# Performance work log

Measured on AMD Instinct MI355X. Metric: run time of the kernel, lower is better.

## Reference

```python
import jax, jax.numpy as jnp
import numpy as np

N = 500_000      # active voxels
G = 128          # grid extent per axis
CIN, COUT = 32, 64
KK = 27          # 3x3x3 kernel offsets
EPS = 1e-5


def setup_inputs() -> dict:
    rng = np.random.default_rng(0)
    # unique active voxel coordinates in a G^3 grid
    lin = rng.choice(G ** 3, size=N, replace=False)
    coords = np.stack(np.unravel_index(lin, (G, G, G)), -1).astype(np.int64)  # [N,3]
    lut = np.full(G ** 3, N, np.int64)  # N == "missing" sentinel
    lut[lin] = np.arange(N)
    offs = np.stack(np.meshgrid(*([np.arange(-1, 2)] * 3), indexing='ij'), -1).reshape(-1, 3)
    nbr = np.full((N, KK), N, np.int64)  # kernel map: nbr[i,k] = input index at coord_i + off_k
    for k, o in enumerate(offs):
        c = coords + o
        valid = np.all((c >= 0) & (c < G), axis=1)
        keys = (c[:, 0] * G + c[:, 1]) * G + c[:, 2]
        nbr[valid, k] = lut[keys[valid]]

    key = jax.random.key(0)
    ks = jax.random.split(key, 4)
    x = jax.random.normal(ks[0], (N, CIN), jnp.float32)
    W1 = jax.random.normal(ks[1], (KK, CIN, COUT), jnp.float32) * (1.0 / np.sqrt(KK * CIN))
    W2 = jax.random.normal(ks[2], (KK, COUT, COUT), jnp.float32) * (1.0 / np.sqrt(KK * COUT))
    Wres = jax.random.normal(ks[3], (CIN, COUT), jnp.float32) * (1.0 / np.sqrt(CIN))
    bres = jnp.zeros((COUT,), jnp.float32)
    g1 = jnp.ones((CIN,), jnp.float32)
    b1 = jnp.zeros((CIN,), jnp.float32)
    g2 = jnp.ones((COUT,), jnp.float32)
    b2 = jnp.zeros((COUT,), jnp.float32)
    return dict(x=x, nbr=jnp.asarray(nbr), W1=W1, W2=W2, Wres=Wres, bres=bres,
                g1=g1, b1=b1, g2=g2, b2=b2)


def _bn(x, g, b):
    # MinkowskiBatchNorm (training mode): stats over all active sites
    m = jnp.mean(x, axis=0)
    v = jnp.var(x, axis=0)
    return (x - m) * jax.lax.rsqrt(v + EPS) * g + b


def _sparse_conv(x, nbr, W):
    # gather-GEMM-scatter sparse conv; x:[N,Cin], nbr:[N,KK], W:[KK,Cin,Cout]
    xp = jnp.concatenate([x, jnp.zeros((1, x.shape[1]), x.dtype)], axis=0)  # sentinel row
    out = jnp.zeros((x.shape[0], W.shape[2]), x.dtype)
    for k in range(W.shape[0]):  # fixed small loop over 27 kernel offsets
        out = out + xp[nbr[:, k]] @ W[k]
    return out


def reference(x, nbr, W1, W2, Wres, bres, g1, b1, g2, b2):
    residual = x @ Wres + bres                               # MinkowskiLinear (in != out)
    out = _sparse_conv(jax.nn.relu(_bn(x, g1, b1)), nbr, W1)   # conv1(act1(norm1(x)))
    out = _sparse_conv(jax.nn.relu(_bn(out, g2, b2)), nbr, W2)  # conv2(act2(norm2(out)))
    return out + residual
```

## Files before the change

### kernel.cpp

```cpp
#include <hip/hip_runtime.h>

#define NVOX 500000
#define CIN 32
#define COUT 64
#define KK 27
#define EPSV 1e-5f

typedef __bf16 bf16x8 __attribute__((ext_vector_type(8)));
typedef float f32x4 __attribute__((ext_vector_type(4)));

#define MFMA16 __builtin_amdgcn_mfma_f32_16x16x32_bf16

__device__ __forceinline__ float bf2f(ushort u) {
    return __uint_as_float(((unsigned)u) << 16);
}
__device__ __forceinline__ ushort f2bf(float f) {
    unsigned u = __float_as_uint(f);
    unsigned r = (u + 0x7FFFu + ((u >> 16) & 1u)) >> 16;
    return (ushort)r;
}
union U4BF { uint4 u; bf16x8 b; ushort s[8]; };
__device__ __forceinline__ bf16x8 as_bf8(uint4 v) { U4BF c; c.u = v; return c.b; }
__device__ __forceinline__ bf16x8 f8_to_bf8(float4 a, float4 b) {
    U4BF c;
    c.s[0] = f2bf(a.x); c.s[1] = f2bf(a.y); c.s[2] = f2bf(a.z); c.s[3] = f2bf(a.w);
    c.s[4] = f2bf(b.x); c.s[5] = f2bf(b.y); c.s[6] = f2bf(b.z); c.s[7] = f2bf(b.w);
    return c.b;
}

__device__ __forceinline__ float4 ldv4(const float4* p, long long i) { return p[i]; }
__device__ __forceinline__ float4 ldv4(const ushort4* p, long long i) {
    ushort4 u = p[i];
    return make_float4(bf2f(u.x), bf2f(u.y), bf2f(u.z), bf2f(u.w));
}

__global__ void prep_kernel(const float* __restrict__ W1, const float* __restrict__ W2,
                            const float* __restrict__ Wres,
                            ushort* __restrict__ w1s, ushort* __restrict__ w2s,
                            ushort* __restrict__ wrs,
                            float* __restrict__ stats,
                            ushort* __restrict__ y1, ushort* __restrict__ y2) {
    int t = blockIdx.x * 256 + threadIdx.x;
    if (t < 192) { stats[t] = 0.f; return; }
    if (t < 224) { y1[(size_t)NVOX * CIN + (t - 192)] = 0; return; }
    if (t < 288) { y2[(size_t)NVOX * COUT + (t - 224)] = 0; return; }
    int d = t - 288;
    if (d < 27 * 4 * 64 * 8) {
        int j = d & 7, lane = (d >> 3) & 63, nt = (d >> 9) & 3, k = d >> 11;
        int ci = ((lane >> 4) << 3) + j, co = (nt << 4) + (lane & 15);
        w1s[d] = f2bf(W1[(k * CIN + ci) * COUT + co]);
        return;
    }
    d -= 27 * 4 * 64 * 8;
    if (d < 27 * 2 * 4 * 64 * 8) {
        int j = d & 7, lane = (d >> 3) & 63, nt = (d >> 9) & 3, half = (d >> 11) & 1, k = d >> 12;
        int ci = (half << 5) + ((lane >> 4) << 3) + j, co = (nt << 4) + (lane & 15);
        w2s[d] = f2bf(W2[(k * COUT + ci) * COUT + co]);
        return;
    }
    d -= 27 * 2 * 4 * 64 * 8;
    if (d < 4 * 64 * 8) {
        int j = d & 7, lane = (d >> 3) & 63, nt = (d >> 9) & 3;
        int ci = ((lane >> 4) << 3) + j, co = (nt << 4) + (lane & 15);
        wrs[d] = f2bf(Wres[ci * COUT + co]);
    }
}

template <int C, typename T4>
__global__ void stats_kernel(const T4* __restrict__ in, long long total4,
                             float* __restrict__ gsum, float* __restrict__ gsq) {
    __shared__ float s_sum[C];
    __shared__ float s_sq[C];
    int t = threadIdx.x;
    if (t < C) { s_sum[t] = 0.f; s_sq[t] = 0.f; }
    __syncthreads();
    long long i0 = (long long)blockIdx.x * blockDim.x + t;
    long long stride = (long long)gridDim.x * blockDim.x;
    int c0 = (int)((i0 * 4) & (C - 1));
    float ls0 = 0.f, ls1 = 0.f, ls2 = 0.f, ls3 = 0.f;
    float lq0 = 0.f, lq1 = 0.f, lq2 = 0.f, lq3 = 0.f;
    for (long long i = i0; i < total4; i += stride) {
        float4 v = ldv4(in, i);
        ls0 += v.x; lq0 += v.x * v.x;
        ls1 += v.y; lq1 += v.y * v.y;
        ls2 += v.z; lq2 += v.z * v.z;
        ls3 += v.w; lq3 += v.w * v.w;
    }
    atomicAdd(&s_sum[c0 + 0], ls0); atomicAdd(&s_sq[c0 + 0], lq0);
    atomicAdd(&s_sum[c0 + 1], ls1); atomicAdd(&s_sq[c0 + 1], lq1);
    atomicAdd(&s_sum[c0 + 2], ls2); atomicAdd(&s_sq[c0 + 2], lq2);
    atomicAdd(&s_sum[c0 + 3], ls3); atomicAdd(&s_sq[c0 + 3], lq3);
    __syncthreads();
    if (t < C) {
        atomicAdd(&gsum[t], s_sum[t]);
        atomicAdd(&gsq[t], s_sq[t]);
    }
}

template <int C, typename T4>
__global__ void bn_relu_kernel(const T4* __restrict__ in, ushort4* __restrict__ out,
                               long long total4,
                               const float* __restrict__ gsum, const float* __restrict__ gsq,
                               const float* __restrict__ gamma, const float* __restrict__ beta,
                               float invN) {
    long long i0 = (long long)blockIdx.x * blockDim.x + threadIdx.x;
    long long stride = (long long)gridDim.x * blockDim.x;
    int c0 = (int)((i0 * 4) & (C - 1));
    float a[4], bb[4];
#pragma unroll
    for (int j = 0; j < 4; j++) {
        int c = c0 + j;
        float m = gsum[c] * invN;
        float v = fmaxf(gsq[c] * invN - m * m, 0.f);
        a[j] = gamma[c] * rsqrtf(v + EPSV);
        bb[j] = beta[c] - m * a[j];
    }
    for (long long i = i0; i < total4; i += stride) {
        float4 v = ldv4(in, i);
        ushort4 o;
        o.x = f2bf(fmaxf(v.x * a[0] + bb[0], 0.f));
        o.y = f2bf(fmaxf(v.y * a[1] + bb[1], 0.f));
        o.z = f2bf(fmaxf(v.z * a[2] + bb[2], 0.f));
        o.w = f2bf(fmaxf(v.w * a[3] + bb[3], 0.f));
        out[i] = o;
    }
}

__global__ __launch_bounds__(256, 4) void conv1_kernel(const ushort* __restrict__ y1,
                                                       const int* __restrict__ nbr,
                                                       const ushort* __restrict__ w1s,
                                                       ushort* __restrict__ out1,
                                                       float* __restrict__ gsum,
                                                       float* __restrict__ gsq) {
    __shared__ int s_idx[192 * KK];
    __shared__ uint4 swb[2][256];
    __shared__ float s_sum[COUT], s_sq[COUT];
    const int tid = threadIdx.x;
    const int lane = tid & 63, wv = tid >> 6;
    const int m = lane & 15, g = lane >> 4;
    if (tid < COUT) { s_sum[tid] = 0.f; s_sq[tid] = 0.f; }

    const int blockRow0 = blockIdx.x * 192;
    const int gbase = blockRow0 * KK;
    const int glim = NVOX * KK;
    for (int i = tid; i < 192 * KK; i += 256) {
        int gi = gbase + i;
        int v = (gi < glim) ? nbr[gi] : NVOX;
        s_idx[i] = (int)min((unsigned)v, (unsigned)NVOX);
    }
    const uint4* __restrict__ w1v = (const uint4*)w1s;
    swb[0][tid] = w1v[tid];
    __syncthreads();

    const uint4* __restrict__ yv = (const uint4*)y1;
    const int ib[3] = {(wv * 48 + m) * KK, (wv * 48 + 16 + m) * KK, (wv * 48 + 32 + m) * KK};

    uint4 ga[3][2];
#pragma unroll
    for (int p = 0; p < 2; p++)
#pragma unroll
        for (int t = 0; t < 3; t++) ga[t][p] = yv[s_idx[ib[t] + p] * 4 + g];

    f32x4 acc[3][4];
#pragma unroll
    for (int t = 0; t < 3; t++)
#pragma unroll
        for (int nt = 0; nt < 4; nt++) acc[t][nt] = (f32x4){0.f, 0.f, 0.f, 0.f};

#pragma unroll
    for (int k = 0; k < KK; k++) {
        const int b = k & 1;
        uint4 wld;
        if (k + 1 < KK) wld = w1v[(k + 1) * 256 + tid];
        __builtin_amdgcn_sched_barrier(0);
        uint4 wb0 = swb[b][lane];
        uint4 wb1 = swb[b][64 + lane];
        uint4 wb2 = swb[b][128 + lane];
        uint4 wb3 = swb[b][192 + lane];
        __builtin_amdgcn_s_setprio(1);
#pragma unroll
        for (int t = 0; t < 3; t++) {
            bf16x8 a = as_bf8(ga[t][b]);
            acc[t][0] = MFMA16(a, as_bf8(wb0), acc[t][0], 0, 0, 0);
            acc[t][1] = MFMA16(a, as_bf8(wb1), acc[t][1], 0, 0, 0);
            acc[t][2] = MFMA16(a, as_bf8(wb2), acc[t][2], 0, 0, 0);
            acc[t][3] = MFMA16(a, as_bf8(wb3), acc[t][3], 0, 0, 0);
        }
        __builtin_amdgcn_s_setprio(0);
        __builtin_amdgcn_sched_barrier(0);
        if (k + 2 < KK) {
#pragma unroll
            for (int t = 0; t < 3; t++) ga[t][b] = yv[s_idx[ib[t] + k + 2] * 4 + g];
        }
        if (k + 1 < KK) {
            swb[b ^ 1][tid] = wld;
            asm volatile("s_waitcnt lgkmcnt(0)" ::: "memory");
            __builtin_amdgcn_s_barrier();
            __builtin_amdgcn_sched_barrier(0);
        }
    }

#pragma unroll
    for (int t = 0; t < 3; t++) {
        int rbase = blockRow0 + wv * 48 + t * 16 + g * 4;
#pragma unroll
        for (int reg = 0; reg < 4; reg++) {
            int r = rbase + reg;
            if (r < NVOX) {
                size_t bo = (size_t)r * COUT + m;
                out1[bo] = f2bf(acc[t][0][reg]);
                out1[bo + 16] = f2bf(acc[t][1][reg]);
                out1[bo + 32] = f2bf(acc[t][2][reg]);
                out1[bo + 48] = f2bf(acc[t][3][reg]);
            }
        }
    }

#pragma unroll
    for (int nt = 0; nt < 4; nt++) {
        float s = 0.f, q = 0.f;
#pragma unroll
        for (int t = 0; t < 3; t++)
#pragma unroll
            for (int reg = 0; reg < 4; reg++) {
                float v = acc[t][nt][reg];
                s += v; q += v * v;
            }
        s += __shfl_xor(s, 16); q += __shfl_xor(q, 16);
        s += __shfl_xor(s, 32); q += __shfl_xor(q, 32);
        if (g == 0) { atomicAdd(&s_sum[nt * 16 + m], s); atomicAdd(&s_sq[nt * 16 + m], q); }
    }
    __syncthreads();
    if (tid < COUT) {
        atomicAdd(&gsum[tid], s_sum[tid]);
        atomicAdd(&gsq[tid], s_sq[tid]);
    }
}

__global__ __launch_bounds__(256, 4) void conv2_kernel(const ushort* __restrict__ y2,
                                                       const int* __restrict__ nbr,
                                                       const ushort* __restrict__ w2s,
                                                       const float* __restrict__ x,
                                                       const ushort* __restrict__ wrs,
                                                       const float* __restrict__ bres,
                                                       float* __restrict__ out) {
    __shared__ int s_idx[128 * KK];
    __shared__ uint4 swb[2][512];
    const int tid = threadIdx.x;
    const int lane = tid & 63, wv = tid >> 6;
    const int m = lane & 15, g = lane >> 4;

    const int blockRow0 = blockIdx.x * 128;
    const int gbase = blockRow0 * KK;
    const int glim = NVOX * KK;
    for (int i = tid; i < 128 * KK; i += 256) {
        int gi = gbase + i;
        int v = (gi < glim) ? nbr[gi] : NVOX;
        s_idx[i] = (int)min((unsigned)v, (unsigned)NVOX);
    }
    const uint4* __restrict__ w2v = (const uint4*)w2s;
    swb[0][tid] = w2v[tid];
    swb[0][256 + tid] = w2v[256 + tid];
    __syncthreads();

    const uint4* __restrict__ yv = (const uint4*)y2;
    const float4* __restrict__ xv = (const float4*)x;
    const uint4* __restrict__ wrv = (const uint4*)wrs;
    const int ib[2] = {(wv * 32 + m) * KK, (wv * 32 + 16 + m) * KK};

    uint4 ga[2][2][2];
#pragma unroll
    for (int p = 0; p < 2; p++)
#pragma unroll
        for (int t = 0; t < 2; t++) {
            int idx = s_idx[ib[t] + p];
            ga[t][0][p] = yv[idx * 8 + g];
            ga[t][1][p] = yv[idx * 8 + 4 + g];
        }

    f32x4 acc[2][4];
#pragma unroll
    for (int t = 0; t < 2; t++)
#pragma unroll
        for (int nt = 0; nt < 4; nt++) acc[t][nt] = (f32x4){0.f, 0.f, 0.f, 0.f};

#pragma unroll
    for (int k = 0; k < KK; k++) {
        const int b = k & 1;
        uint4 wld0, wld1;
        if (k + 1 < KK) {
            wld0 = w2v[(k + 1) * 512 + tid];
            wld1 = w2v[(k + 1) * 512 + 256 + tid];
        }
        __builtin_amdgcn_sched_barrier(0);
        uint4 wb0 = swb[b][lane];
        uint4 wb1 = swb[b][64 + lane];
        uint4 wb2 = swb[b][128 + lane];
        uint4 wb3 = swb[b][192 + lane];
        __builtin_amdgcn_s_setprio(1);
#pragma unroll
        for (int t = 0; t < 2; t++) {
            bf16x8 a0 = as_bf8(ga[t][0][b]);
            acc[t][0] = MFMA16(a0, as_bf8(wb0), acc[t][0], 0, 0, 0);
            acc[t][1] = MFMA16(a0, as_bf8(wb1), acc[t][1], 0, 0, 0);
            acc[t][2] = MFMA16(a0, as_bf8(wb2), acc[t][2], 0, 0, 0);
            acc[t][3] = MFMA16(a0, as_bf8(wb3), acc[t][3], 0, 0, 0);
        }
        __builtin_amdgcn_s_setprio(0);
        uint4 wb4 = swb[b][256 + lane];
        uint4 wb5 = swb[b][320 + lane];
        uint4 wb6 = swb[b][384 + lane];
        uint4 wb7 = swb[b][448 + lane];
        __builtin_amdgcn_s_setprio(1);
#pragma unroll
        for (int t = 0; t < 2; t++) {
            bf16x8 a1 = as_bf8(ga[t][1][b]);
            acc[t][0] = MFMA16(a1, as_bf8(wb4), acc[t][0], 0, 0, 0);
            acc[t][1] = MFMA16(a1, as_bf8(wb5), acc[t][1], 0, 0, 0);
            acc[t][2] = MFMA16(a1, as_bf8(wb6), acc[t][2], 0, 0, 0);
            acc[t][3] = MFMA16(a1, as_bf8(wb7), acc[t][3], 0, 0, 0);
        }
        __builtin_amdgcn_s_setprio(0);
        __builtin_amdgcn_sched_barrier(0);
        if (k + 2 < KK) {
#pragma unroll
            for (int t = 0; t < 2; t++) {
                int idx = s_idx[ib[t] + k + 2];
                ga[t][0][b] = yv[idx * 8 + g];
                ga[t][1][b] = yv[idx * 8 + 4 + g];
            }
        }
        if (k + 1 < KK) {
            swb[b ^ 1][tid] = wld0;
            swb[b ^ 1][256 + tid] = wld1;
            asm volatile("s_waitcnt lgkmcnt(0)" ::: "memory");
            __builtin_amdgcn_s_barrier();
            __builtin_amdgcn_sched_barrier(0);
        }
    }

    uint4 wr0 = wrv[lane];
    uint4 wr1 = wrv[64 + lane];
    uint4 wr2 = wrv[128 + lane];
    uint4 wr3 = wrv[192 + lane];
#pragma unroll
    for (int t = 0; t < 2; t++) {
        int arow = blockRow0 + wv * 32 + t * 16 + m;
        bf16x8 ar;
        if (arow < NVOX) {
            float4 f0 = xv[(size_t)arow * 8 + g * 2];
            float4 f1 = xv[(size_t)arow * 8 + g * 2 + 1];
            ar = f8_to_bf8(f0, f1);
        } else {
            uint4 zz = {0u, 0u, 0u, 0u};
            ar = as_bf8(zz);
        }
        acc[t][0] = MFMA16(ar, as_bf8(wr0), acc[t][0], 0, 0, 0);
        acc[t][1] = MFMA16(ar, as_bf8(wr1), acc[t][1], 0, 0, 0);
        acc[t][2] = MFMA16(ar, as_bf8(wr2), acc[t][2], 0, 0, 0);
        acc[t][3] = MFMA16(ar, as_bf8(wr3), acc[t][3], 0, 0, 0);
    }

    float br0 = bres[m];
    float br1 = bres[16 + m];
    float br2 = bres[32 + m];
    float br3 = bres[48 + m];
#pragma unroll
    for (int t = 0; t < 2; t++) {
        int rbase = blockRow0 + wv * 32 + t * 16 + g * 4;
#pragma unroll
        for (int reg = 0; reg < 4; reg++) {
            int r = rbase + reg;
            if (r < NVOX) {
                size_t bo = (size_t)r * COUT + m;
                out[bo] = acc[t][0][reg] + br0;
                out[bo + 16] = acc[t][1][reg] + br1;
                out[bo + 32] = acc[t][2][reg] + br2;
                out[bo + 48] = acc[t][3][reg] + br3;
            }
        }
    }
}

extern "C" void kernel_launch(void* const* d_in, const int* in_sizes, int n_in,
                              void* d_out, int out_size, void* d_ws, size_t ws_size,
                              hipStream_t stream) {
    const float* x = (const float*)d_in[0];
    const int* nbr = (const int*)d_in[1];
    const float* W1 = (const float*)d_in[2];
    const float* W2 = (const float*)d_in[3];
    const float* Wres = (const float*)d_in[4];
    const float* bres = (const float*)d_in[5];
    const float* g1 = (const float*)d_in[6];
    const float* b1 = (const float*)d_in[7];
    const float* g2 = (const float*)d_in[8];
    const float* b2 = (const float*)d_in[9];
    float* out = (float*)d_out;

    char* ws = (char*)d_ws;
    size_t off = 0;
    auto alloc = [&](size_t bytes) -> void* {
        void* p = ws + off;
        off = (off + bytes + 255) & ~(size_t)255;
        return p;
    };
    ushort* y1 = (ushort*)alloc((size_t)(NVOX + 1) * CIN * 2);
    ushort* y2 = (ushort*)alloc((size_t)(NVOX + 1) * COUT * 2);
    ushort* w1s = (ushort*)alloc(55296 * 2);
    ushort* w2s = (ushort*)alloc(110592 * 2);
    ushort* wrs = (ushort*)alloc(2048 * 2);
    float* stats = (float*)alloc(192 * 4);
    float* sum1 = stats, *sq1 = stats + 32, *sum2 = stats + 64, *sq2 = stats + 128;
    ushort* out1 = (ushort*)d_out;

    const float invN = 1.0f / (float)NVOX;
    const long long tot1 = (long long)NVOX * CIN / 4;
    const long long tot2 = (long long)NVOX * COUT / 4;
    const int conv1Grid = (NVOX + 191) / 192;
    const int conv2Grid = (NVOX + 127) / 128;

    hipLaunchKernelGGL(prep_kernel, dim3(658), dim3(256), 0, stream,
                       W1, W2, Wres, w1s, w2s, wrs, stats, y1, y2);
    hipLaunchKernelGGL(HIP_KERNEL_NAME(stats_kernel<32, float4>), dim3(1024), dim3(256), 0, stream,
                       (const float4*)x, tot1, sum1, sq1);
    hipLaunchKernelGGL(HIP_KERNEL_NAME(bn_relu_kernel<32, float4>), dim3(2048), dim3(256), 0, stream,
                       (const float4*)x, (ushort4*)y1, tot1, sum1, sq1, g1, b1, invN);
    hipLaunchKernelGGL(conv1_kernel, dim3(conv1Grid), dim3(256), 0, stream,
                       y1, nbr, w1s, out1, sum2, sq2);
    hipLaunchKernelGGL(HIP_KERNEL_NAME(bn_relu_kernel<64, ushort4>), dim3(2048), dim3(256), 0, stream,
                       (const ushort4*)out1, (ushort4*)y2, tot2, sum2, sq2, g2, b2, invN);
    hipLaunchKernelGGL(conv2_kernel, dim3(conv2Grid), dim3(256), 0, stream,
                       y2, nbr, w2s, x, wrs, bres, out);
    (void)in_sizes; (void)n_in; (void)out_size; (void)ws_size;
}
```

Baseline: 544.9 us.

## Load conv weights directly from global/L2 instead of double-buffered LDS with barriers

Both sparse-conv kernels drop the shared-memory double buffer for the per-offset weight slices. Each wave now reads its weight fragments straight from global memory, which removes one block-wide barrier and an LDS store per kernel offset. Neighbor indices are also read from LDS one offset ahead into registers, so the gather address is ready early. The cost is that every wave issues its own global weight loads, relying on cache hits, and those loads now sit on the MFMA critical path with no explicit prefetch.

```diff
diff --git a/kernel.cpp b/kernel.cpp
--- a/kernel.cpp
+++ b/kernel.cpp
@@ -133,7 +133,6 @@
                                                        float* __restrict__ gsum,
                                                        float* __restrict__ gsq) {
     __shared__ int s_idx[192 * KK];
-    __shared__ uint4 swb[2][256];
     __shared__ float s_sum[COUT], s_sq[COUT];
     const int tid = threadIdx.x;
     const int lane = tid & 63, wv = tid >> 6;
@@ -148,18 +147,20 @@
         int v = (gi < glim) ? nbr[gi] : NVOX;
         s_idx[i] = (int)min((unsigned)v, (unsigned)NVOX);
     }
+    __syncthreads();
+
+    const uint4* __restrict__ yv = (const uint4*)y1;
     const uint4* __restrict__ w1v = (const uint4*)w1s;
-    swb[0][tid] = w1v[tid];
-    __syncthreads();
-
-    const uint4* __restrict__ yv = (const uint4*)y1;
     const int ib[3] = {(wv * 48 + m) * KK, (wv * 48 + 16 + m) * KK, (wv * 48 + 32 + m) * KK};
 
     uint4 ga[3][2];
+    int ni[3];
 #pragma unroll
     for (int p = 0; p < 2; p++)
 #pragma unroll
         for (int t = 0; t < 3; t++) ga[t][p] = yv[s_idx[ib[t] + p] * 4 + g];
+#pragma unroll
+    for (int t = 0; t < 3; t++) ni[t] = s_idx[ib[t] + 2];
 
     f32x4 acc[3][4];
 #pragma unroll
@@ -170,13 +171,10 @@
 #pragma unroll
     for (int k = 0; k < KK; k++) {
         const int b = k & 1;
-        uint4 wld;
-        if (k + 1 < KK) wld = w1v[(k + 1) * 256 + tid];
-        __builtin_amdgcn_sched_barrier(0);
-        uint4 wb0 = swb[b][lane];
-        uint4 wb1 = swb[b][64 + lane];
-        uint4 wb2 = swb[b][128 + lane];
-        uint4 wb3 = swb[b][192 + lane];
+        uint4 wb0 = w1v[(k * 4 + 0) * 64 + lane];
+        uint4 wb1 = w1v[(k * 4 + 1) * 64 + lane];
+        uint4 wb2 = w1v[(k * 4 + 2) * 64 + lane];
+        uint4 wb3 = w1v[(k * 4 + 3) * 64 + lane];
         __builtin_amdgcn_s_setprio(1);
 #pragma unroll
         for (int t = 0; t < 3; t++) {
@@ -190,14 +188,13 @@
         __builtin_amdgcn_sched_barrier(0);
         if (k + 2 < KK) {
 #pragma unroll
-            for (int t = 0; t < 3; t++) ga[t][b] = yv[s_idx[ib[t] + k + 2] * 4 + g];
-        }
-        if (k + 1 < KK) {
-            swb[b ^ 1][tid] = wld;
-            asm volatile("s_waitcnt lgkmcnt(0)" ::: "memory");
-            __builtin_amdgcn_s_barrier();
-            __builtin_amdgcn_sched_barrier(0);
-        }
+            for (int t = 0; t < 3; t++) ga[t][b] = yv[ni[t] * 4 + g];
+            if (k + 3 < KK) {
+#pragma unroll
+                for (int t = 0; t < 3; t++) ni[t] = s_idx[ib[t] + k + 3];
+            }
+        }
+        __builtin_amdgcn_sched_barrier(0);
     }
 
 #pragma unroll
@@ -245,7 +242,6 @@
                                                        const float* __restrict__ bres,
                                                        float* __restrict__ out) {
     __shared__ int s_idx[128 * KK];
-    __shared__ uint4 swb[2][512];
     const int tid = threadIdx.x;
     const int lane = tid & 63, wv = tid >> 6;
     const int m = lane & 15, g = lane >> 4;
@@ -258,17 +254,16 @@
         int v = (gi < glim) ? nbr[gi] : NVOX;
         s_idx[i] = (int)min((unsigned)v, (unsigned)NVOX);
     }
+    __syncthreads();
+
+    const uint4* __restrict__ yv = (const uint4*)y2;
     const uint4* __restrict__ w2v = (const uint4*)w2s;
-    swb[0][tid] = w2v[tid];
-    swb[0][256 + tid] = w2v[256 + tid];
-    __syncthreads();
-
-    const uint4* __restrict__ yv = (const uint4*)y2;
     const float4* __restrict__ xv = (const float4*)x;
     const uint4* __restrict__ wrv = (const uint4*)wrs;
     const int ib[2] = {(wv * 32 + m) * KK, (wv * 32 + 16 + m) * KK};
 
     uint4 ga[2][2][2];
+    int ni[2];
 #pragma unroll
     for (int p = 0; p < 2; p++)
 #pragma unroll
@@ -277,6 +272,8 @@
             ga[t][0][p] = yv[idx * 8 + g];
             ga[t][1][p] = yv[idx * 8 + 4 + g];
         }
+#pragma unroll
+    for (int t = 0; t < 2; t++) ni[t] = s_idx[ib[t] + 2];
 
     f32x4 acc[2][4];
 #pragma unroll
@@ -287,34 +284,23 @@
 #pragma unroll
     for (int k = 0; k < KK; k++) {
         const int b = k & 1;
-        uint4 wld0, wld1;
-        if (k + 1 < KK) {
-            wld0 = w2v[(k + 1) * 512 + tid];
-            wld1 = w2v[(k + 1) * 512 + 256 + tid];
-        }
-        __builtin_amdgcn_sched_barrier(0);
-        uint4 wb0 = swb[b][lane];
-        uint4 wb1 = swb[b][64 + lane];
-        uint4 wb2 = swb[b][128 + lane];
-        uint4 wb3 = swb[b][192 + lane];
+        uint4 wb0 = w2v[(k * 8 + 0) * 64 + lane];
+        uint4 wb1 = w2v[(k * 8 + 1) * 64 + lane];
+        uint4 wb2 = w2v[(k * 8 + 2) * 64 + lane];
+        uint4 wb3 = w2v[(k * 8 + 3) * 64 + lane];
+        uint4 wb4 = w2v[(k * 8 + 4) * 64 + lane];
+        uint4 wb5 = w2v[(k * 8 + 5) * 64 + lane];
+        uint4 wb6 = w2v[(k * 8 + 6) * 64 + lane];
+        uint4 wb7 = w2v[(k * 8 + 7) * 64 + lane];
         __builtin_amdgcn_s_setprio(1);
 #pragma unroll
         for (int t = 0; t < 2; t++) {
             bf16x8 a0 = as_bf8(ga[t][0][b]);
+            bf16x8 a1 = as_bf8(ga[t][1][b]);
             acc[t][0] = MFMA16(a0, as_bf8(wb0), acc[t][0], 0, 0, 0);
             acc[t][1] = MFMA16(a0, as_bf8(wb1), acc[t][1], 0, 0, 0);
             acc[t][2] = MFMA16(a0, as_bf8(wb2), acc[t][2], 0, 0, 0);
             acc[t][3] = MFMA16(a0, as_bf8(wb3), acc[t][3], 0, 0, 0);
-        }
-        __builtin_amdgcn_s_setprio(0);
-        uint4 wb4 = swb[b][256 + lane];
-        uint4 wb5 = swb[b][320 + lane];
-        uint4 wb6 = swb[b][384 + lane];
-        uint4 wb7 = swb[b][448 + lane];
-        __builtin_amdgcn_s_setprio(1);
-#pragma unroll
-        for (int t = 0; t < 2; t++) {
-            bf16x8 a1 = as_bf8(ga[t][1][b]);
             acc[t][0] = MFMA16(a1, as_bf8(wb4), acc[t][0], 0, 0, 0);
             acc[t][1] = MFMA16(a1, as_bf8(wb5), acc[t][1], 0, 0, 0);
             acc[t][2] = MFMA16(a1, as_bf8(wb6), acc[t][2], 0, 0, 0);
@@ -325,18 +311,15 @@
         if (k + 2 < KK) {
 #pragma unroll
             for (int t = 0; t < 2; t++) {
-                int idx = s_idx[ib[t] + k + 2];
-                ga[t][0][b] = yv[idx * 8 + g];
-                ga[t][1][b] = yv[idx * 8 + 4 + g];
-            }
-        }
-        if (k + 1 < KK) {
-            swb[b ^ 1][tid] = wld0;
-            swb[b ^ 1][256 + tid] = wld1;
-            asm volatile("s_waitcnt lgkmcnt(0)" ::: "memory");
-            __builtin_amdgcn_s_barrier();
-            __builtin_amdgcn_sched_barrier(0);
-        }
+                ga[t][0][b] = yv[ni[t] * 8 + g];
+                ga[t][1][b] = yv[ni[t] * 8 + 4 + g];
+            }
+            if (k + 3 < KK) {
+#pragma unroll
+                for (int t = 0; t < 2; t++) ni[t] = s_idx[ib[t] + k + 3];
+            }
+        }
+        __builtin_amdgcn_sched_barrier(0);
     }
 
     uint4 wr0 = wrv[lane];
```

Result: slower. 627.2 us (+15.1%).

## Stream conv weights via direct global-to-LDS loads and enlarge conv2 row tiles

Applied to the files above, without the earlier changes.

Weight slices for both sparse convolutions are now copied straight from global memory into LDS with global_load_lds. This replaces staging through registers and an explicit LDS store, and synchronisation now uses vmcnt waits that leave the gather loads for the next offset in flight. Conv2 also grows from 128 to 192 rows per block (48 rows per wave), so each weight slice loaded into LDS is reused across more rows. The larger tile raises register and LDS use and lowers the occupancy bound from 4 to 3 blocks. The hand-counted vmcnt values must match the exact number of loads issued, or the kernels will read stale data.

```diff
diff --git a/kernel.cpp b/kernel.cpp
--- a/kernel.cpp
+++ b/kernel.cpp
@@ -26,6 +26,12 @@
     c.s[0] = f2bf(a.x); c.s[1] = f2bf(a.y); c.s[2] = f2bf(a.z); c.s[3] = f2bf(a.w);
     c.s[4] = f2bf(b.x); c.s[5] = f2bf(b.y); c.s[6] = f2bf(b.z); c.s[7] = f2bf(b.w);
     return c.b;
+}
+
+__device__ __forceinline__ void dma16(const uint4* g, uint4* l) {
+    __builtin_amdgcn_global_load_lds(
+        (const __attribute__((address_space(1))) unsigned int*)g,
+        (__attribute__((address_space(3))) unsigned int*)l, 16, 0, 0);
 }
 
 __device__ __forceinline__ float4 ldv4(const float4* p, long long i) { return p[i]; }
@@ -140,6 +146,9 @@
     const int m = lane & 15, g = lane >> 4;
     if (tid < COUT) { s_sum[tid] = 0.f; s_sq[tid] = 0.f; }
 
+    const uint4* __restrict__ w1v = (const uint4*)w1s;
+    dma16(w1v + tid, &swb[0][wv * 64]);
+
     const int blockRow0 = blockIdx.x * 192;
     const int gbase = blockRow0 * KK;
     const int glim = NVOX * KK;
@@ -148,8 +157,6 @@
         int v = (gi < glim) ? nbr[gi] : NVOX;
         s_idx[i] = (int)min((unsigned)v, (unsigned)NVOX);
     }
-    const uint4* __restrict__ w1v = (const uint4*)w1s;
-    swb[0][tid] = w1v[tid];
     __syncthreads();
 
     const uint4* __restrict__ yv = (const uint4*)y1;
@@ -170,8 +177,8 @@
 #pragma unroll
     for (int k = 0; k < KK; k++) {
         const int b = k & 1;
-        uint4 wld;
-        if (k + 1 < KK) wld = w1v[(k + 1) * 256 + tid];
+        if (k + 1 < KK)
+            dma16(w1v + (k + 1) * 256 + tid, &swb[b ^ 1][wv * 64]);
         __builtin_amdgcn_sched_barrier(0);
         uint4 wb0 = swb[b][lane];
         uint4 wb1 = swb[b][64 + lane];
@@ -192,9 +199,10 @@
 #pragma unroll
             for (int t = 0; t < 3; t++) ga[t][b] = yv[s_idx[ib[t] + k + 2] * 4 + g];
         }
+        __builtin_amdgcn_sched_barrier(0);
         if (k + 1 < KK) {
-            swb[b ^ 1][tid] = wld;
-            asm volatile("s_waitcnt lgkmcnt(0)" ::: "memory");
+            if (k + 2 < KK) asm volatile("s_waitcnt vmcnt(3)" ::: "memory");
+            else            asm volatile("s_waitcnt vmcnt(0)" ::: "memory");
             __builtin_amdgcn_s_barrier();
             __builtin_amdgcn_sched_barrier(0);
         }
@@ -237,60 +245,60 @@
     }
 }
 
-__global__ __launch_bounds__(256, 4) void conv2_kernel(const ushort* __restrict__ y2,
+__global__ __launch_bounds__(256, 3) void conv2_kernel(const ushort* __restrict__ y2,
                                                        const int* __restrict__ nbr,
                                                        const ushort* __restrict__ w2s,
                                                        const float* __restrict__ x,
                                                        const ushort* __restrict__ wrs,
                                                        const float* __restrict__ bres,
                                                        float* __restrict__ out) {
-    __shared__ int s_idx[128 * KK];
+    __shared__ int s_idx[192 * KK];
     __shared__ uint4 swb[2][512];
     const int tid = threadIdx.x;
     const int lane = tid & 63, wv = tid >> 6;
     const int m = lane & 15, g = lane >> 4;
 
-    const int blockRow0 = blockIdx.x * 128;
+    const uint4* __restrict__ w2v = (const uint4*)w2s;
+    dma16(w2v + tid, &swb[0][wv * 64]);
+    dma16(w2v + 256 + tid, &swb[0][256 + wv * 64]);
+
+    const int blockRow0 = blockIdx.x * 192;
     const int gbase = blockRow0 * KK;
     const int glim = NVOX * KK;
-    for (int i = tid; i < 128 * KK; i += 256) {
+    for (int i = tid; i < 192 * KK; i += 256) {
         int gi = gbase + i;
         int v = (gi < glim) ? nbr[gi] : NVOX;
         s_idx[i] = (int)min((unsigned)v, (unsigned)NVOX);
     }
-    const uint4* __restrict__ w2v = (const uint4*)w2s;
-    swb[0][tid] = w2v[tid];
-    swb[0][256 + tid] = w2v[256 + tid];
     __syncthreads();
 
     const uint4* __restrict__ yv = (const uint4*)y2;
     const float4* __restrict__ xv = (const float4*)x;
     const uint4* __restrict__ wrv = (const uint4*)wrs;
-    const int ib[2] = {(wv * 32 + m) * KK, (wv * 32 + 16 + m) * KK};
-
-    uint4 ga[2][2][2];
+    const int ib[3] = {(wv * 48 + m) * KK, (wv * 48 + 16 + m) * KK, (wv * 48 + 32 + m) * KK};
+
+    uint4 ga[3][2][2];
 #pragma unroll
     for (int p = 0; p < 2; p++)
 #pragma unroll
-        for (int t = 0; t < 2; t++) {
+        for (int t = 0; t < 3; t++) {
             int idx = s_idx[ib[t] + p];
             ga[t][0][p] = yv[idx * 8 + g];
             ga[t][1][p] = yv[idx * 8 + 4 + g];
         }
 
-    f32x4 acc[2][4];
-#pragma unroll
-    for (int t = 0; t < 2; t++)
+    f32x4 acc[3][4];
+#pragma unroll
+    for (int t = 0; t < 3; t++)
 #pragma unroll
         for (int nt = 0; nt < 4; nt++) acc[t][nt] = (f32x4){0.f, 0.f, 0.f, 0.f};
 
 #pragma unroll
     for (int k = 0; k < KK; k++) {
         const int b = k & 1;
-        uint4 wld0, wld1;
         if (k + 1 < KK) {
-            wld0 = w2v[(k + 1) * 512 + tid];
-            wld1 = w2v[(k + 1) * 512 + 256 + tid];
+            dma16(w2v + (k + 1) * 512 + tid, &swb[b ^ 1][wv * 64]);
+            dma16(w2v + (k + 1) * 512 + 256 + tid, &swb[b ^ 1][256 + wv * 64]);
         }
         __builtin_amdgcn_sched_barrier(0);
         uint4 wb0 = swb[b][lane];
@@ -299,7 +307,7 @@
         uint4 wb3 = swb[b][192 + lane];
         __builtin_amdgcn_s_setprio(1);
 #pragma unroll
-        for (int t = 0; t < 2; t++) {
+        for (int t = 0; t < 3; t++) {
             bf16x8 a0 = as_bf8(ga[t][0][b]);
             acc[t][0] = MFMA16(a0, as_bf8(wb0), acc[t][0], 0, 0, 0);
             acc[t][1] = MFMA16(a0, as_bf8(wb1), acc[t][1], 0, 0, 0);
@@ -313,7 +321,7 @@
         uint4 wb7 = swb[b][448 + lane];
         __builtin_amdgcn_s_setprio(1);
 #pragma unroll
-        for (int t = 0; t < 2; t++) {
+        for (int t = 0; t < 3; t++) {
             bf16x8 a1 = as_bf8(ga[t][1][b]);
             acc[t][0] = MFMA16(a1, as_bf8(wb4), acc[t][0], 0, 0, 0);
             acc[t][1] = MFMA16(a1, as_bf8(wb5), acc[t][1], 0, 0, 0);
@@ -324,16 +332,16 @@
         __builtin_amdgcn_sched_barrier(0);
         if (k + 2 < KK) {
 #pragma unroll
-            for (int t = 0; t < 2; t++) {
+            for (int t = 0; t < 3; t++) {
                 int idx = s_idx[ib[t] + k + 2];
                 ga[t][0][b] = yv[idx * 8 + g];
                 ga[t][1][b] = yv[idx * 8 + 4 + g];
             }
         }
+        __builtin_amdgcn_sched_barrier(0);
         if (k + 1 < KK) {
-            swb[b ^ 1][tid] = wld0;
-            swb[b ^ 1][256 + tid] = wld1;
-            asm volatile("s_waitcnt lgkmcnt(0)" ::: "memory");
+            if (k + 2 < KK) asm volatile("s_waitcnt vmcnt(6)" ::: "memory");
+            else            asm volatile("s_waitcnt vmcnt(0)" ::: "memory");
             __builtin_amdgcn_s_barrier();
             __builtin_amdgcn_sched_barrier(0);
         }
@@ -344,8 +352,8 @@
     uint4 wr2 = wrv[128 + lane];
     uint4 wr3 = wrv[192 + lane];
 #pragma unroll
-    for (int t = 0; t < 2; t++) {
-        int arow = blockRow0 + wv * 32 + t * 16 + m;
+    for (int t = 0; t < 3; t++) {
+        int arow = blockRow0 + wv * 48 + t * 16 + m;
         bf16x8 ar;
         if (arow < NVOX) {
             float4 f0 = xv[(size_t)arow * 8 + g * 2];
@@ -366,8 +374,8 @@
     float br2 = bres[32 + m];
     float br3 = bres[48 + m];
 #pragma unroll
-    for (int t = 0; t < 2; t++) {
-        int rbase = blockRow0 + wv * 32 + t * 16 + g * 4;
+    for (int t = 0; t < 3; t++) {
+        int rbase = blockRow0 + wv * 48 + t * 16 + g * 4;
 #pragma unroll
         for (int reg = 0; reg < 4; reg++) {
             int r = rbase + reg;
@@ -417,7 +425,7 @@
     const long long tot1 = (long long)NVOX * CIN / 4;
     const long long tot2 = (long long)NVOX * COUT / 4;
     const int conv1Grid = (NVOX + 191) / 192;
-    const int conv2Grid = (NVOX + 127) / 128;
+    const int conv2Grid = (NVOX + 191) / 192;
 
     hipLaunchKernelGGL(prep_kernel, dim3(658), dim3(256), 0, stream,
                        W1, W2, Wres, w1s, w2s, wrs, stats, y1, y2);
```

Result: slower. 564.7 us (+3.6%).
